# Performance work log

Measured on AMD Instinct MI355X. Metric: run time of the kernel, lower is better.

Reference implementation:

```python
import jax, jax.numpy as jnp
import numpy as np

N_NODES = 100000
N_EDGES = 1600000
IN_DIM, HID_DIM, OUT_DIM = 128, 128, 64


def setup_inputs() -> dict:
    key = jax.random.key(0)
    k1, k2, k3, k4 = jax.random.split(key, 4)
    x = jax.random.normal(k1, (N_NODES, IN_DIM), dtype=jnp.float32)
    edge_index = jax.random.randint(k2, (2, N_EDGES), 0, N_NODES, dtype=jnp.int64)
    W1 = jax.random.normal(k3, (IN_DIM, HID_DIM), dtype=jnp.float32) * (1.0 / np.sqrt(IN_DIM))
    b1 = jnp.zeros((HID_DIM,), dtype=jnp.float32)
    W2 = jax.random.normal(k4, (HID_DIM, OUT_DIM), dtype=jnp.float32) * (1.0 / np.sqrt(HID_DIM))
    b2 = jnp.zeros((OUT_DIM,), dtype=jnp.float32)
    return {"x": x, "edge_index": edge_index, "W1": W1, "b1": b1, "W2": W2, "b2": b2}


def _gcn_conv(h, src, dst, norm, W, b, n_nodes):
    # Dense transform first (PyG GCNConv order), then gather-scatter aggregation.
    h = h @ W                                   # [N, out]
    msg = h[src] * norm[:, None]                # [E, out] gather + scale
    out = jax.ops.segment_sum(msg, dst, num_segments=n_nodes)  # scatter-add
    return out + b


def reference(x, edge_index, W1, b1, W2, b2):
    src, dst = edge_index[0], edge_index[1]
    n = x.shape[0]
    # symmetric normalization: deg from in-degree (unit edge weights), no self loops
    deg = jax.ops.segment_sum(jnp.ones_like(src, dtype=x.dtype), dst, num_segments=n)
    deg_inv_sqrt = jnp.where(deg > 0, jax.lax.rsqrt(jnp.maximum(deg, 1.0)), 0.0)
    norm = deg_inv_sqrt[src] * deg_inv_sqrt[dst]  # [E]
    h = jax.nn.relu(_gcn_conv(x, src, dst, norm, W1, b1, n))
    # dropout is identity in eval mode
    out = _gcn_conv(h, src, dst, norm, W2, b2, n)
    return out
```

## Files before the change

### kernel.cpp

```cpp
#include <hip/hip_runtime.h>
#include <stdint.h>

#define NN 100000
#define NE 1600000
#define K_DIM 128

#define BSH 7
#define NBKT ((NN + (1 << BSH) - 1) >> BSH)
#define EPT 32
#define BIN_CHUNK (256 * EPT)
#define CAP 4096
#define PADE 2400000

typedef unsigned int uint32;
typedef unsigned short ushort16;
typedef __attribute__((ext_vector_type(8))) short bf16x8;
typedef __attribute__((ext_vector_type(4))) float f32x4;

__device__ __forceinline__ ushort16 f2bf(float f) {
    uint32 u = __float_as_uint(f);
    u += 0x7fffu + ((u >> 16) & 1u);
    return (ushort16)(u >> 16);
}
__device__ __forceinline__ float bf_lo(uint32 u) { return __uint_as_float(u << 16); }
__device__ __forceinline__ float bf_hi(uint32 u) { return __uint_as_float(u & 0xffff0000u); }

__device__ __forceinline__ bf16x8 ld_frag8(const ushort16* p) {
    uint2 lo = *(const uint2*)p;
    uint2 hi = *(const uint2*)(p + 4);
    union { uint32 u[4]; bf16x8 v; } x;
    x.u[0] = lo.x; x.u[1] = lo.y; x.u[2] = hi.x; x.u[3] = hi.y;
    return x.v;
}


__global__ __launch_bounds__(256) void bin_pass1_kernel(
        const int* __restrict__ ei, int* __restrict__ gcursor,
        uint2* __restrict__ staging) {
    __shared__ int hist[NBKT];
    __shared__ int base[NBKT];
    int tid = threadIdx.x;
    int e0 = blockIdx.x * BIN_CHUNK;

    for (int i = tid; i < NBKT; i += 256) hist[i] = 0;
    __syncthreads();

    #pragma unroll
    for (int k = 0; k < EPT; k++) {
        int e = e0 + k * 256 + tid;
        if (e < NE) {
            int d = ei[NE + e];
            atomicAdd(&hist[d >> BSH], 1);
        }
    }
    __syncthreads();

    for (int i = tid; i < NBKT; i += 256) {
        int c = hist[i];
        base[i] = c ? atomicAdd(&gcursor[i], c) : 0;
        hist[i] = 0;
    }
    __syncthreads();

    #pragma unroll
    for (int k = 0; k < EPT; k++) {
        int e = e0 + k * 256 + tid;
        if (e < NE) {
            int s = ei[e];
            int d = ei[NE + e];
            int b = d >> BSH;
            int off = atomicAdd(&hist[b], 1);
            staging[(size_t)b * CAP + base[b] + off] = make_uint2((uint32)s, (uint32)d);
        }
    }
}

__global__ __launch_bounds__(256) void deg_bucket_kernel(
        const uint2* __restrict__ staging, const int* __restrict__ gcursor,
        int* __restrict__ deg, float* __restrict__ dis, int* __restrict__ bucket_tot) {
    __shared__ int cnt[1 << BSH];
    __shared__ int red[1 << BSH];
    int b = blockIdx.x;
    int node0 = b << BSH;
    int tid = threadIdx.x;
    int n_edges = gcursor[b];

    if (tid < (1 << BSH)) cnt[tid] = 0;
    __syncthreads();

    for (int i = tid; i < n_edges; i += 256) {
        uint2 p = staging[(size_t)b * CAP + i];
        atomicAdd(&cnt[p.y & ((1 << BSH) - 1)], 1);
    }
    __syncthreads();

    if (tid < (1 << BSH)) {
        int node = node0 + tid;
        int c = cnt[tid];
        if (node < NN) {
            deg[node] = c;
            dis[node] = (c > 0) ? rsqrtf((float)c) : 0.0f;
            red[tid] = (c + 7) & ~7;
        } else {
            red[tid] = 0;
        }
    }
    __syncthreads();
    for (int off = (1 << BSH) / 2; off > 0; off >>= 1) {
        if (tid < off) red[tid] += red[tid + off];
        __syncthreads();
    }
    if (tid == 0) bucket_tot[b] = red[0];
}

__global__ void bucket_scan_kernel(const int* __restrict__ bucket_tot,
                                   int* __restrict__ bucket_base,
                                   int* __restrict__ row_start) {
    __shared__ int buf[1024];
    int tid = threadIdx.x;
    int v = (tid < NBKT) ? bucket_tot[tid] : 0;
    buf[tid] = v;
    __syncthreads();
    for (int off = 1; off < 1024; off <<= 1) {
        int t = (tid >= off) ? buf[tid - off] : 0;
        __syncthreads();
        buf[tid] += t;
        __syncthreads();
    }
    if (tid < NBKT) bucket_base[tid] = buf[tid] - v;
    if (tid == NBKT - 1) row_start[NN] = buf[tid];
}

__global__ __launch_bounds__(256) void bin_pass2_kernel(
        const uint2* __restrict__ staging, const int* __restrict__ gcursor,
        const int* __restrict__ deg, const int* __restrict__ bucket_base,
        int* __restrict__ row_start, int* __restrict__ ssrc) {
    __shared__ int sb[1 << BSH];
    __shared__ int cur[1 << BSH];
    __shared__ int pend[1 << BSH];
    int b = blockIdx.x;
    int node0 = b << BSH;
    int tid = threadIdx.x;
    int n_edges = gcursor[b];

    int p = 0;
    if (tid < (1 << BSH)) {
        int node = node0 + tid;
        p = (node < NN) ? ((deg[node] + 7) & ~7) : 0;
        sb[tid] = p;
    }
    __syncthreads();
    #pragma unroll
    for (int off = 1; off < (1 << BSH); off <<= 1) {
        int t = (tid >= off && tid < (1 << BSH)) ? sb[tid - off] : 0;
        __syncthreads();
        if (tid < (1 << BSH)) sb[tid] += t;
        __syncthreads();
    }
    if (tid < (1 << BSH)) {
        int rs = bucket_base[b] + sb[tid] - p;
        cur[tid] = rs;
        pend[tid] = rs + p;
        int node = node0 + tid;
        if (node < NN) row_start[node] = rs;
    }
    __syncthreads();

    for (int i = tid; i < n_edges; i += 256) {
        uint2 pr = staging[(size_t)b * CAP + i];
        int off = atomicAdd(&cur[pr.y & ((1 << BSH) - 1)], 1);
        ssrc[off] = (int)pr.x;
    }
    __syncthreads();

    if (tid < (1 << BSH)) {
        int node = node0 + tid;
        if (node < NN) {
            for (int q = cur[tid]; q < pend[tid]; q++) ssrc[q] = NN;
        }
    }
}

template <int N, bool ABF16>
__global__ __launch_bounds__(256) void gemm_mfma_kernel(
        const void* __restrict__ Ap, const float* __restrict__ W,
        const float* __restrict__ dis, ushort16* __restrict__ out, int M) {
    constexpr int BM = 64, K = K_DIM;
    constexpr int LDA = 132;
    constexpr int NT = N / 16;
    constexpr int NLOG = (N == 128) ? 7 : 6;

    __shared__ ushort16 As[BM * LDA];
    __shared__ ushort16 Bt[N * LDA];

    int tid = threadIdx.x;
    int row0 = blockIdx.x * BM;

    if constexpr (!ABF16) {
        const float* A = (const float*)Ap;
        #pragma unroll
        for (int c = 0; c < 8; c++) {
            int idx = c * 1024 + tid * 4;
            int r = idx >> 7, col = idx & 127;
            int ra = row0 + r;
            float4 v = (ra < M) ? *(const float4*)&A[(size_t)ra * K + col]
                                : make_float4(0.f, 0.f, 0.f, 0.f);
            ushort4 bq;
            bq.x = f2bf(v.x); bq.y = f2bf(v.y); bq.z = f2bf(v.z); bq.w = f2bf(v.w);
            *(ushort4*)&As[r * LDA + col] = bq;
        }
    } else {
        const ushort16* A = (const ushort16*)Ap;
        #pragma unroll
        for (int c = 0; c < 4; c++) {
            int idx = c * 2048 + tid * 8;
            int r = idx >> 7, col = idx & 127;
            int ra = row0 + r;
            uint4 v = make_uint4(0u, 0u, 0u, 0u);
            if (ra < M) v = *(const uint4*)&A[(size_t)ra * K + col];
            *(uint2*)&As[r * LDA + col]     = make_uint2(v.x, v.y);
            *(uint2*)&As[r * LDA + col + 4] = make_uint2(v.z, v.w);
        }
    }
    {
        #pragma unroll
        for (int c = 0; c < (K * N) / 1024; c++) {
            int idx = c * 1024 + tid * 4;
            int k = idx >> NLOG, n = idx & (N - 1);
            float4 v = *(const float4*)&W[idx];
            Bt[(n + 0) * LDA + k] = f2bf(v.x);
            Bt[(n + 1) * LDA + k] = f2bf(v.y);
            Bt[(n + 2) * LDA + k] = f2bf(v.z);
            Bt[(n + 3) * LDA + k] = f2bf(v.w);
        }
    }
    __syncthreads();

    int lane = tid & 63;
    int wv = tid >> 6;
    int m0 = wv * 16;
    int ml = lane & 15;
    int quad = lane >> 4;

    f32x4 acc[NT];
    #pragma unroll
    for (int i = 0; i < NT; i++) acc[i] = (f32x4){0.f, 0.f, 0.f, 0.f};

    #pragma unroll
    for (int ks = 0; ks < 4; ks++) {
        int kof = ks * 32 + quad * 8;
        bf16x8 a = ld_frag8(&As[(m0 + ml) * LDA + kof]);
        #pragma unroll
        for (int nt = 0; nt < NT; nt++) {
            bf16x8 bb = ld_frag8(&Bt[(nt * 16 + ml) * LDA + kof]);
            acc[nt] = __builtin_amdgcn_mfma_f32_16x16x32_bf16(a, bb, acc[nt], 0, 0, 0);
        }
    }

    #pragma unroll
    for (int r = 0; r < 4; r++) {
        int row = row0 + m0 + quad * 4 + r;
        if (row < M) {
            float s = dis[row];
            #pragma unroll
            for (int nt = 0; nt < NT; nt++)
                out[(size_t)row * N + nt * 16 + ml] = f2bf(acc[nt][r] * s);
        }
    }
}

__global__ __launch_bounds__(256) void agg128_kernel(
        const ushort16* __restrict__ g, const int* __restrict__ row_start,
        const int* __restrict__ ssrc, const float* __restrict__ dis,
        const float* __restrict__ bias, ushort16* __restrict__ out) {
    int wave = (blockIdx.x * 256 + threadIdx.x) >> 6;
    int lane = threadIdx.x & 63;
    if (wave >= NN) return;

    int beg = row_start[wave];
    int end = row_start[wave + 1];
    float sc = dis[wave];

    float ax = 0.f, ay = 0.f;
    for (int e = beg; e < end; e += 8) {
        int idx = ssrc[e + (lane & 7)];
        #pragma unroll
        for (int j = 0; j < 8; j++) {
            int s = __shfl(idx, j);
            uint32 u = *(const uint32*)&g[(size_t)s * 128 + lane * 2];
            ax += bf_lo(u);
            ay += bf_hi(u);
        }
    }
    float2 b = *(const float2*)&bias[lane * 2];
    float ox = fmaxf(sc * ax + b.x, 0.f);
    float oy = fmaxf(sc * ay + b.y, 0.f);
    uint32 pk = ((uint32)f2bf(oy) << 16) | (uint32)f2bf(ox);
    *(uint32*)&out[(size_t)wave * 128 + lane * 2] = pk;
}

__global__ __launch_bounds__(256) void agg64_kernel(
        const ushort16* __restrict__ g, const int* __restrict__ row_start,
        const int* __restrict__ ssrc, const float* __restrict__ dis,
        const float* __restrict__ bias, float* __restrict__ out) {
    int wave = (blockIdx.x * 256 + threadIdx.x) >> 6;
    int lane = threadIdx.x & 63;
    int half = lane >> 5;
    int l2 = lane & 31;
    int node = wave * 2 + half;
    if (node >= NN) return;

    int beg = row_start[node];
    int end = row_start[node + 1];
    float sc = dis[node];

    float ax = 0.f, ay = 0.f;
    for (int e = beg; e < end; e += 8) {
        int idx = ssrc[e + (l2 & 7)];
        #pragma unroll
        for (int j = 0; j < 8; j++) {
            int s = __shfl(idx, half * 32 + j);
            uint32 u = *(const uint32*)&g[(size_t)s * 64 + l2 * 2];
            ax += bf_lo(u);
            ay += bf_hi(u);
        }
    }
    float2 b = *(const float2*)&bias[l2 * 2];
    *(float2*)&out[(size_t)node * 64 + l2 * 2] =
        make_float2(sc * ax + b.x, sc * ay + b.y);
}

extern "C" void kernel_launch(void* const* d_in, const int* in_sizes, int n_in,
                              void* d_out, int out_size, void* d_ws, size_t ws_size,
                              hipStream_t stream) {
    const float* x  = (const float*)d_in[0];
    const int*   ei = (const int*)d_in[1];
    const float* W1 = (const float*)d_in[2];
    const float* b1 = (const float*)d_in[3];
    const float* W2 = (const float*)d_in[4];
    const float* b2 = (const float*)d_in[5];
    float* out = (float*)d_out;

    char* ws = (char*)d_ws;
    size_t off = 0;
    auto alloc = [&](size_t bytes) {
        void* p = ws + off;
        off = (off + bytes + 255) & ~(size_t)255;
        return p;
    };

    int*      deg_i      = (int*)alloc(NN * 4);
    float*    dis        = (float*)alloc(NN * 4);
    int*      row_start  = (int*)alloc((NN + 1) * 4);
    int*      gcursor    = (int*)alloc(NBKT * 4);
    int*      bucket_tot = (int*)alloc(NBKT * 4);
    int*      bucket_bse = (int*)alloc(NBKT * 4);
    int*      ssrc       = (int*)alloc((size_t)PADE * 4);
    ushort16* g1         = (ushort16*)alloc((size_t)(NN + 1) * 128 * 2);
    char*     big        = (char*)alloc((size_t)NBKT * CAP * 8);
    uint2*    staging    = (uint2*)big;
    ushort16* h          = (ushort16*)big;
    ushort16* g2         = g1;

    hipMemsetAsync(gcursor, 0, NBKT * 4, stream);
    hipMemsetAsync((char*)g1 + (size_t)NN * 256, 0, 256, stream);

    bin_pass1_kernel<<<(NE + BIN_CHUNK - 1) / BIN_CHUNK, 256, 0, stream>>>(ei, gcursor, staging);
    deg_bucket_kernel<<<NBKT, 256, 0, stream>>>(staging, gcursor, deg_i, dis, bucket_tot);
    bucket_scan_kernel<<<1, 1024, 0, stream>>>(bucket_tot, bucket_bse, row_start);
    bin_pass2_kernel<<<NBKT, 256, 0, stream>>>(staging, gcursor, deg_i, bucket_bse, row_start, ssrc);

    const int GEMM_BLOCKS = (NN + 63) / 64;
    gemm_mfma_kernel<128, false><<<GEMM_BLOCKS, 256, 0, stream>>>(x, W1, dis, g1, NN);

    const int AGG_BLOCKS = (NN + 3) / 4;
    agg128_kernel<<<AGG_BLOCKS, 256, 0, stream>>>(g1, row_start, ssrc, dis, b1, h);

    hipMemsetAsync((char*)g2 + (size_t)NN * 128, 0, 128, stream);

    gemm_mfma_kernel<64, true><<<GEMM_BLOCKS, 256, 0, stream>>>(h, W2, dis, g2, NN);

    const int AGG2_BLOCKS = (NN / 2 + 3) / 4;
    agg64_kernel<<<AGG2_BLOCKS, 256, 0, stream>>>(g2, row_start, ssrc, dis, b2, out);
}
```

Baseline: 278.7 us.

## Fuse CSR build into one kernel and widen aggregation gathers to 16-byte loads

Merges the degree count, bucket scan and second binning pass into one kernel that places each bucket's CSR segment at a fixed per-bucket offset (b*CAP). This needs separate row_start/row_end arrays and drops the global scan and two launches. Both aggregation kernels now gather 8 bf16 values per lane with uint4 loads, handle several edges in parallel across lane groups, and combine partial sums with xor shuffles. The layer-2 aggregation uses a full wave per node instead of a half-wave. The cost is a larger, sparser ssrc array, extra shuffle reductions, and idle lanes at the final store.

```diff
diff --git a/kernel.cpp b/kernel.cpp
--- a/kernel.cpp
+++ b/kernel.cpp
@@ -10,7 +10,6 @@
 #define EPT 32
 #define BIN_CHUNK (256 * EPT)
 #define CAP 4096
-#define PADE 2400000
 
 typedef unsigned int uint32;
 typedef unsigned short ushort16;
@@ -24,6 +23,13 @@
 }
 __device__ __forceinline__ float bf_lo(uint32 u) { return __uint_as_float(u << 16); }
 __device__ __forceinline__ float bf_hi(uint32 u) { return __uint_as_float(u & 0xffff0000u); }
+
+__device__ __forceinline__ void acc8(float* acc, uint4 v) {
+    acc[0] += bf_lo(v.x); acc[1] += bf_hi(v.x);
+    acc[2] += bf_lo(v.y); acc[3] += bf_hi(v.y);
+    acc[4] += bf_lo(v.z); acc[5] += bf_hi(v.z);
+    acc[6] += bf_lo(v.w); acc[7] += bf_hi(v.w);
+}
 
 __device__ __forceinline__ bf16x8 ld_frag8(const ushort16* p) {
     uint2 lo = *(const uint2*)p;
@@ -75,66 +81,11 @@
     }
 }
 
-__global__ __launch_bounds__(256) void deg_bucket_kernel(
+__global__ __launch_bounds__(256) void csr_build_kernel(
         const uint2* __restrict__ staging, const int* __restrict__ gcursor,
-        int* __restrict__ deg, float* __restrict__ dis, int* __restrict__ bucket_tot) {
+        float* __restrict__ dis, int* __restrict__ row_start, int* __restrict__ row_end,
+        int* __restrict__ ssrc) {
     __shared__ int cnt[1 << BSH];
-    __shared__ int red[1 << BSH];
-    int b = blockIdx.x;
-    int node0 = b << BSH;
-    int tid = threadIdx.x;
-    int n_edges = gcursor[b];
-
-    if (tid < (1 << BSH)) cnt[tid] = 0;
-    __syncthreads();
-
-    for (int i = tid; i < n_edges; i += 256) {
-        uint2 p = staging[(size_t)b * CAP + i];
-        atomicAdd(&cnt[p.y & ((1 << BSH) - 1)], 1);
-    }
-    __syncthreads();
-
-    if (tid < (1 << BSH)) {
-        int node = node0 + tid;
-        int c = cnt[tid];
-        if (node < NN) {
-            deg[node] = c;
-            dis[node] = (c > 0) ? rsqrtf((float)c) : 0.0f;
-            red[tid] = (c + 7) & ~7;
-        } else {
-            red[tid] = 0;
-        }
-    }
-    __syncthreads();
-    for (int off = (1 << BSH) / 2; off > 0; off >>= 1) {
-        if (tid < off) red[tid] += red[tid + off];
-        __syncthreads();
-    }
-    if (tid == 0) bucket_tot[b] = red[0];
-}
-
-__global__ void bucket_scan_kernel(const int* __restrict__ bucket_tot,
-                                   int* __restrict__ bucket_base,
-                                   int* __restrict__ row_start) {
-    __shared__ int buf[1024];
-    int tid = threadIdx.x;
-    int v = (tid < NBKT) ? bucket_tot[tid] : 0;
-    buf[tid] = v;
-    __syncthreads();
-    for (int off = 1; off < 1024; off <<= 1) {
-        int t = (tid >= off) ? buf[tid - off] : 0;
-        __syncthreads();
-        buf[tid] += t;
-        __syncthreads();
-    }
-    if (tid < NBKT) bucket_base[tid] = buf[tid] - v;
-    if (tid == NBKT - 1) row_start[NN] = buf[tid];
-}
-
-__global__ __launch_bounds__(256) void bin_pass2_kernel(
-        const uint2* __restrict__ staging, const int* __restrict__ gcursor,
-        const int* __restrict__ deg, const int* __restrict__ bucket_base,
-        int* __restrict__ row_start, int* __restrict__ ssrc) {
     __shared__ int sb[1 << BSH];
     __shared__ int cur[1 << BSH];
     __shared__ int pend[1 << BSH];
@@ -143,10 +94,19 @@
     int tid = threadIdx.x;
     int n_edges = gcursor[b];
 
+    if (tid < (1 << BSH)) cnt[tid] = 0;
+    __syncthreads();
+
+    for (int i = tid; i < n_edges; i += 256) {
+        uint2 p = staging[(size_t)b * CAP + i];
+        atomicAdd(&cnt[p.y & ((1 << BSH) - 1)], 1);
+    }
+    __syncthreads();
+
     int p = 0;
     if (tid < (1 << BSH)) {
         int node = node0 + tid;
-        p = (node < NN) ? ((deg[node] + 7) & ~7) : 0;
+        p = (node < NN) ? ((cnt[tid] + 7) & ~7) : 0;
         sb[tid] = p;
     }
     __syncthreads();
@@ -158,11 +118,16 @@
         __syncthreads();
     }
     if (tid < (1 << BSH)) {
-        int rs = bucket_base[b] + sb[tid] - p;
+        int rs = b * CAP + sb[tid] - p;
         cur[tid] = rs;
         pend[tid] = rs + p;
         int node = node0 + tid;
-        if (node < NN) row_start[node] = rs;
+        if (node < NN) {
+            row_start[node] = rs;
+            row_end[node] = rs + p;
+            int c = cnt[tid];
+            dis[node] = (c > 0) ? rsqrtf((float)c) : 0.0f;
+        }
     }
     __syncthreads();
 
@@ -271,63 +236,95 @@
 
 __global__ __launch_bounds__(256) void agg128_kernel(
         const ushort16* __restrict__ g, const int* __restrict__ row_start,
-        const int* __restrict__ ssrc, const float* __restrict__ dis,
-        const float* __restrict__ bias, ushort16* __restrict__ out) {
+        const int* __restrict__ row_end, const int* __restrict__ ssrc,
+        const float* __restrict__ dis, const float* __restrict__ bias,
+        ushort16* __restrict__ out) {
     int wave = (blockIdx.x * 256 + threadIdx.x) >> 6;
     int lane = threadIdx.x & 63;
     if (wave >= NN) return;
 
+    int f = lane & 15;
+    int gq = lane >> 4;
+
     int beg = row_start[wave];
-    int end = row_start[wave + 1];
+    int end = row_end[wave];
     float sc = dis[wave];
 
-    float ax = 0.f, ay = 0.f;
+    float acc[8] = {};
     for (int e = beg; e < end; e += 8) {
         int idx = ssrc[e + (lane & 7)];
         #pragma unroll
-        for (int j = 0; j < 8; j++) {
-            int s = __shfl(idx, j);
-            uint32 u = *(const uint32*)&g[(size_t)s * 128 + lane * 2];
-            ax += bf_lo(u);
-            ay += bf_hi(u);
-        }
-    }
-    float2 b = *(const float2*)&bias[lane * 2];
-    float ox = fmaxf(sc * ax + b.x, 0.f);
-    float oy = fmaxf(sc * ay + b.y, 0.f);
-    uint32 pk = ((uint32)f2bf(oy) << 16) | (uint32)f2bf(ox);
-    *(uint32*)&out[(size_t)wave * 128 + lane * 2] = pk;
+        for (int j = 0; j < 2; j++) {
+            int s = __shfl(idx, gq * 2 + j);
+            uint4 v = *(const uint4*)&g[(size_t)s * 128 + f * 8];
+            acc8(acc, v);
+        }
+    }
+    #pragma unroll
+    for (int i = 0; i < 8; i++) {
+        acc[i] += __shfl_xor(acc[i], 16);
+        acc[i] += __shfl_xor(acc[i], 32);
+    }
+    if (gq == 0) {
+        float4 b0 = *(const float4*)&bias[f * 8];
+        float4 b1 = *(const float4*)&bias[f * 8 + 4];
+        float o0 = fmaxf(sc * acc[0] + b0.x, 0.f);
+        float o1 = fmaxf(sc * acc[1] + b0.y, 0.f);
+        float o2 = fmaxf(sc * acc[2] + b0.z, 0.f);
+        float o3 = fmaxf(sc * acc[3] + b0.w, 0.f);
+        float o4 = fmaxf(sc * acc[4] + b1.x, 0.f);
+        float o5 = fmaxf(sc * acc[5] + b1.y, 0.f);
+        float o6 = fmaxf(sc * acc[6] + b1.z, 0.f);
+        float o7 = fmaxf(sc * acc[7] + b1.w, 0.f);
+        uint4 pk;
+        pk.x = ((uint32)f2bf(o1) << 16) | (uint32)f2bf(o0);
+        pk.y = ((uint32)f2bf(o3) << 16) | (uint32)f2bf(o2);
+        pk.z = ((uint32)f2bf(o5) << 16) | (uint32)f2bf(o4);
+        pk.w = ((uint32)f2bf(o7) << 16) | (uint32)f2bf(o6);
+        *(uint4*)&out[(size_t)wave * 128 + f * 8] = pk;
+    }
 }
 
 __global__ __launch_bounds__(256) void agg64_kernel(
         const ushort16* __restrict__ g, const int* __restrict__ row_start,
-        const int* __restrict__ ssrc, const float* __restrict__ dis,
-        const float* __restrict__ bias, float* __restrict__ out) {
+        const int* __restrict__ row_end, const int* __restrict__ ssrc,
+        const float* __restrict__ dis, const float* __restrict__ bias,
+        float* __restrict__ out) {
     int wave = (blockIdx.x * 256 + threadIdx.x) >> 6;
     int lane = threadIdx.x & 63;
-    int half = lane >> 5;
-    int l2 = lane & 31;
-    int node = wave * 2 + half;
-    if (node >= NN) return;
-
-    int beg = row_start[node];
-    int end = row_start[node + 1];
-    float sc = dis[node];
-
-    float ax = 0.f, ay = 0.f;
+    if (wave >= NN) return;
+
+    int f = lane & 7;
+    int gq = lane >> 3;
+
+    int beg = row_start[wave];
+    int end = row_end[wave];
+    float sc = dis[wave];
+
+    float acc[8] = {};
     for (int e = beg; e < end; e += 8) {
-        int idx = ssrc[e + (l2 & 7)];
-        #pragma unroll
-        for (int j = 0; j < 8; j++) {
-            int s = __shfl(idx, half * 32 + j);
-            uint32 u = *(const uint32*)&g[(size_t)s * 64 + l2 * 2];
-            ax += bf_lo(u);
-            ay += bf_hi(u);
-        }
-    }
-    float2 b = *(const float2*)&bias[l2 * 2];
-    *(float2*)&out[(size_t)node * 64 + l2 * 2] =
-        make_float2(sc * ax + b.x, sc * ay + b.y);
+        int idx = ssrc[e + (lane & 7)];
+        int s = __shfl(idx, gq);
+        uint4 v = *(const uint4*)&g[(size_t)s * 64 + f * 8];
+        acc8(acc, v);
+    }
+    #pragma unroll
+    for (int i = 0; i < 8; i++) {
+        acc[i] += __shfl_xor(acc[i], 8);
+        acc[i] += __shfl_xor(acc[i], 16);
+        acc[i] += __shfl_xor(acc[i], 32);
+    }
+    if (gq == 0) {
+        float4 b0 = *(const float4*)&bias[f * 8];
+        float4 b1 = *(const float4*)&bias[f * 8 + 4];
+        float4 o0, o1;
+        o0.x = sc * acc[0] + b0.x; o0.y = sc * acc[1] + b0.y;
+        o0.z = sc * acc[2] + b0.z; o0.w = sc * acc[3] + b0.w;
+        o1.x = sc * acc[4] + b1.x; o1.y = sc * acc[5] + b1.y;
+        o1.z = sc * acc[6] + b1.z; o1.w = sc * acc[7] + b1.w;
+        *(float4*)&out[(size_t)wave * 64 + f * 8] = o0;
+        *(float4*)&out[(size_t)wave * 64 + f * 8 + 4] = o1;
+    }
 }
 
 extern "C" void kernel_launch(void* const* d_in, const int* in_sizes, int n_in,
@@ -349,13 +346,11 @@
         return p;
     };
 
-    int*      deg_i      = (int*)alloc(NN * 4);
     float*    dis        = (float*)alloc(NN * 4);
-    int*      row_start  = (int*)alloc((NN + 1) * 4);
+    int*      row_start  = (int*)alloc(NN * 4);
+    int*      row_end    = (int*)alloc(NN * 4);
     int*      gcursor    = (int*)alloc(NBKT * 4);
-    int*      bucket_tot = (int*)alloc(NBKT * 4);
-    int*      bucket_bse = (int*)alloc(NBKT * 4);
-    int*      ssrc       = (int*)alloc((size_t)PADE * 4);
+    int*      ssrc       = (int*)alloc((size_t)NBKT * CAP * 4);
     ushort16* g1         = (ushort16*)alloc((size_t)(NN + 1) * 128 * 2);
     char*     big        = (char*)alloc((size_t)NBKT * CAP * 8);
     uint2*    staging    = (uint2*)big;
@@ -366,20 +361,17 @@
     hipMemsetAsync((char*)g1 + (size_t)NN * 256, 0, 256, stream);
 
     bin_pass1_kernel<<<(NE + BIN_CHUNK - 1) / BIN_CHUNK, 256, 0, stream>>>(ei, gcursor, staging);
-    deg_bucket_kernel<<<NBKT, 256, 0, stream>>>(staging, gcursor, deg_i, dis, bucket_tot);
-    bucket_scan_kernel<<<1, 1024, 0, stream>>>(bucket_tot, bucket_bse, row_start);
-    bin_pass2_kernel<<<NBKT, 256, 0, stream>>>(staging, gcursor, deg_i, bucket_bse, row_start, ssrc);
+    csr_build_kernel<<<NBKT, 256, 0, stream>>>(staging, gcursor, dis, row_start, row_end, ssrc);
 
     const int GEMM_BLOCKS = (NN + 63) / 64;
     gemm_mfma_kernel<128, false><<<GEMM_BLOCKS, 256, 0, stream>>>(x, W1, dis, g1, NN);
 
     const int AGG_BLOCKS = (NN + 3) / 4;
-    agg128_kernel<<<AGG_BLOCKS, 256, 0, stream>>>(g1, row_start, ssrc, dis, b1, h);
+    agg128_kernel<<<AGG_BLOCKS, 256, 0, stream>>>(g1, row_start, row_end, ssrc, dis, b1, h);
 
     hipMemsetAsync((char*)g2 + (size_t)NN * 128, 0, 128, stream);
 
     gemm_mfma_kernel<64, true><<<GEMM_BLOCKS, 256, 0, stream>>>(h, W2, dis, g2, NN);
 
-    const int AGG2_BLOCKS = (NN / 2 + 3) / 4;
-    agg64_kernel<<<AGG2_BLOCKS, 256, 0, stream>>>(g2, row_start, ssrc, dis, b2, out);
-}
+    agg64_kernel<<<AGG_BLOCKS, 256, 0, stream>>>(g2, row_start, row_end, ssrc, dis, b2, out);
+}
```

Measured after the change: 288.0 us. 1.03x slower.
